# Kernel optimization log

Measured on AMD Instinct MI355X. Metric: run time of the kernel, lower is better.

The kernel has to match this reference:

```python
import jax, jax.numpy as jnp
import numpy as np

NUM_CLASSES = 1000
FEATURE_DIM = 1024
BATCH = 8192
MOMENTUM = 0.9
LAMBDA_INTRA = 1.0
LAMBDA_INTER = 0.5


def setup_inputs() -> dict:
    key = jax.random.key(0)
    k1, k2, k3, k4 = jax.random.split(key, 4)
    return {
        "features": jax.random.normal(k1, (BATCH, FEATURE_DIM), jnp.float32),
        "features_adv": jax.random.normal(k2, (BATCH, FEATURE_DIM), jnp.float32),
        "centers": jax.random.normal(k3, (NUM_CLASSES, FEATURE_DIM), jnp.float32),
        "labels": jax.random.randint(k4, (BATCH,), 0, NUM_CLASSES, dtype=jnp.int64),
    }


def _l2_normalize(x):
    # torch F.normalize(p=2, dim=1) with eps=1e-12 clamp on the norm
    n = jnp.linalg.norm(x, axis=1, keepdims=True)
    return x / jnp.maximum(n, 1e-12)


def _update_centers(centers, feats, labels):
    # Vectorized version of the per-class masked-mean momentum update.
    C = centers.shape[0]
    sums = jax.ops.segment_sum(feats, labels, num_segments=C)            # [C, D]
    counts = jax.ops.segment_sum(jnp.ones((feats.shape[0],), feats.dtype), labels, num_segments=C)  # [C]
    means = sums / jnp.maximum(counts, 1.0)[:, None]
    has_samples = (counts > 0)[:, None]
    center_is_zero = jnp.all(centers == 0, axis=1, keepdims=True)
    updated = jnp.where(center_is_zero, means, MOMENTUM * centers + (1.0 - MOMENTUM) * means)
    return jnp.where(has_samples, updated, centers)


def reference(features, features_adv, centers, labels):
    f = _l2_normalize(features)
    fa = _l2_normalize(features_adv)

    # update_centers runs under no_grad on detached normalized features
    centers_new = _update_centers(centers, jax.lax.stop_gradient(f), labels)

    centers_batch = centers_new[labels]  # [B, D] gather
    intra_clean = jnp.linalg.norm(f - centers_batch, axis=1).mean()
    intra_adv = jnp.linalg.norm(fa - centers_batch, axis=1).mean()

    # fused pairwise center distances: ||ci||^2 + ||cj||^2 - 2 ci.cj
    sq = jnp.sum(centers_new * centers_new, axis=1)                      # [C]
    d2 = sq[:, None] + sq[None, :] - 2.0 * (centers_new @ centers_new.T)  # [C, C]
    dist = jnp.sqrt(jnp.maximum(d2, 0.0))
    C = centers_new.shape[0]
    upper = jnp.triu(jnp.ones((C, C), dtype=bool), k=1)
    n_pairs = C * (C - 1) / 2.0
    inter_loss = jnp.sum(jnp.where(upper, jax.nn.relu(1.0 - dist), 0.0)) / n_pairs

    return LAMBDA_INTRA * (intra_clean + intra_adv) - LAMBDA_INTER * inter_loss
```

## Files before the change

kernel.cpp:

```cpp
#include <hip/hip_runtime.h>
#include <math.h>

#define BATCH 8192
#define DIM 1024
#define NCLS 1000
#define NPAD 1024
#define NPAIRS 499500.0f
#define INTER_TILES 136
#define MAXROWS 128

typedef float  f32x4  __attribute__((ext_vector_type(4)));
typedef short  bf16x8 __attribute__((ext_vector_type(8)));


__device__ inline float waveAllReduceAdd(float x) {
  #pragma unroll
  for (int m = 32; m > 0; m >>= 1) x += __shfl_xor(x, m);
  return x;
}

__device__ inline float blockReduce1(float x, float* sm) {
  x = waveAllReduceAdd(x);
  int lane = threadIdx.x & 63, wid = threadIdx.x >> 6;
  __syncthreads();
  if (lane == 0) sm[wid] = x;
  __syncthreads();
  return sm[0] + sm[1] + sm[2] + sm[3];
}

__device__ inline unsigned short f2bf(float f) {
  unsigned int u = __float_as_uint(f);
  u += 0x7FFFu + ((u >> 16) & 1u);
  return (unsigned short)(u >> 16);
}

__device__ inline void gload_lds16(const float* g, float* l) {
  __builtin_amdgcn_global_load_lds(
      (const __attribute__((address_space(1))) void*)g,
      (__attribute__((address_space(3))) void*)l, 16, 0, 0);
}

__device__ inline void waitvm0() {
  asm volatile("s_waitcnt vmcnt(0)" ::: "memory");
}

__device__ inline void cfence() { asm volatile("" ::: "memory"); }


__global__ __launch_bounds__(256, 4)
void center_intra_kernel(const float* __restrict__ feats,
                         const float* __restrict__ featsa,
                         const float* __restrict__ centers,
                         const int* __restrict__ labels,
                         unsigned short* __restrict__ centers_bf,
                         float* __restrict__ sqn,
                         float* __restrict__ pclean,
                         float* __restrict__ padv) {
  __shared__ float  s_stage[4][DIM];
  __shared__ float4 s_accf[4][256];
  __shared__ float4 s_c4[256];
  __shared__ float  s_iw[MAXROWS];
  __shared__ int    s_rows[MAXROWS];
  __shared__ int    s_cnt;
  __shared__ int    s_anynz;
  __shared__ float  sm[8];

  int c = blockIdx.x;
  int tid = threadIdx.x;
  int lane = tid & 63, w = tid >> 6;
  int fi = tid;

  if (c >= NCLS) {
    ((ushort4*)(centers_bf + (size_t)c * DIM))[fi] = make_ushort4(0, 0, 0, 0);
    return;
  }

  if (tid == 0) { s_cnt = 0; s_anynz = 0; }
  __syncthreads();
  #pragma unroll 4
  for (int j = tid; j < BATCH; j += 256) {
    if (labels[j] == c) {
      int p = atomicAdd(&s_cnt, 1);
      if (p < MAXROWS) s_rows[p] = j;
    }
  }
  __syncthreads();
  int n = min(s_cnt, MAXROWS);

  float4 acc[4];
  #pragma unroll
  for (int i = 0; i < 4; ++i) acc[i] = make_float4(0.f, 0.f, 0.f, 0.f);
  float* myst = s_stage[w];

  for (int t = w; t < n; t += 4) {
    int r = s_rows[t];
    const float* src = feats + (size_t)r * DIM;
    #pragma unroll
    for (int q = 0; q < 4; ++q)
      gload_lds16(src + q * 256 + lane * 4, myst + q * 256);
    waitvm0();
    float4 v[4];
    #pragma unroll
    for (int i = 0; i < 4; ++i) v[i] = ((const float4*)myst)[lane + 64 * i];
    float ss = 0.f;
    #pragma unroll
    for (int i = 0; i < 4; ++i)
      ss += v[i].x * v[i].x + v[i].y * v[i].y + v[i].z * v[i].z + v[i].w * v[i].w;
    ss = waveAllReduceAdd(ss);
    float iw = 1.0f / fmaxf(sqrtf(ss), 1e-12f);
    if (lane == 0) s_iw[t] = iw;
    #pragma unroll
    for (int i = 0; i < 4; ++i) {
      acc[i].x += v[i].x * iw; acc[i].y += v[i].y * iw;
      acc[i].z += v[i].z * iw; acc[i].w += v[i].w * iw;
    }
    cfence();
  }

  #pragma unroll
  for (int i = 0; i < 4; ++i) s_accf[w][lane + 64 * i] = acc[i];
  float4 cv = ((const float4*)(centers + (size_t)c * DIM))[fi];
  if (cv.x != 0.f || cv.y != 0.f || cv.z != 0.f || cv.w != 0.f) s_anynz = 1;
  __syncthreads();
  float4 a0 = s_accf[0][fi], a1 = s_accf[1][fi], a2 = s_accf[2][fi], a3 = s_accf[3][fi];
  float4 sum = make_float4(a0.x + a1.x + a2.x + a3.x, a0.y + a1.y + a2.y + a3.y,
                           a0.z + a1.z + a2.z + a3.z, a0.w + a1.w + a2.w + a3.w);

  float invc = 1.0f / fmaxf((float)n, 1.0f);
  float4 mean = make_float4(sum.x * invc, sum.y * invc, sum.z * invc, sum.w * invc);

  float4 o;
  if (s_anynz) {
    o = make_float4(0.9f * cv.x + 0.1f * mean.x, 0.9f * cv.y + 0.1f * mean.y,
                    0.9f * cv.z + 0.1f * mean.z, 0.9f * cv.w + 0.1f * mean.w);
  } else {
    o = mean;
  }
  if (n == 0) o = cv;

  ((ushort4*)(centers_bf + (size_t)c * DIM))[fi] =
      make_ushort4(f2bf(o.x), f2bf(o.y), f2bf(o.z), f2bf(o.w));
  s_c4[fi] = o;

  float sq = blockReduce1(o.x * o.x + o.y * o.y + o.z * o.z + o.w * o.w, sm);
  if (tid == 0) sqn[c] = sq;

  float sumc = 0.f, suma = 0.f;
  for (int t = w; t < n; t += 4) {
    int r = s_rows[t];
    const float4* rp = (const float4*)(feats  + (size_t)r * DIM);
    const float4* ap = (const float4*)(featsa + (size_t)r * DIM);
    float dotf = 0.f, dota = 0.f, ssa = 0.f;
    #pragma unroll
    for (int i = 0; i < 4; ++i) {
      float4 vf = rp[lane + 64 * i];
      float4 va = ap[lane + 64 * i];
      float4 cc = s_c4[lane + 64 * i];
      dotf += vf.x * cc.x + vf.y * cc.y + vf.z * cc.z + vf.w * cc.w;
      dota += va.x * cc.x + va.y * cc.y + va.z * cc.z + va.w * cc.w;
      ssa  += va.x * va.x + va.y * va.y + va.z * va.z + va.w * va.w;
    }
    dotf = waveAllReduceAdd(dotf);
    dota = waveAllReduceAdd(dota);
    ssa  = waveAllReduceAdd(ssa);
    if (lane == 0) {
      float iw = s_iw[t];
      float inva = 1.0f / fmaxf(sqrtf(ssa), 1e-12f);
      float d2c = 1.0f + sq - 2.0f * iw * dotf;
      float d2a = 1.0f + sq - 2.0f * inva * dota;
      sumc += sqrtf(fmaxf(d2c, 0.0f));
      suma += sqrtf(fmaxf(d2a, 0.0f));
    }
  }

  float totc = blockReduce1(sumc, sm);
  float tota = blockReduce1(suma, sm);
  if (tid == 0) { pclean[c] = totc; padv[c] = tota; }
}


__global__ __launch_bounds__(256, 4)
void inter_mfma_kernel(const unsigned short* __restrict__ Cbf,
                       const float* __restrict__ sq,
                       float* __restrict__ pinter) {
  __shared__ float smr[8];
  int tid = threadIdx.x;
  int bid = blockIdx.x;

  int t = bid;
  int bi = 0;
  while (t >= 16 - bi) { t -= 16 - bi; ++bi; }
  int bj = bi + t;

  int w = tid >> 6;
  int wy = w >> 1, wx = w & 1;
  int lane = tid & 63;
  int m = lane & 15;
  int q = lane >> 4;

  int i0 = bi * 64 + wy * 32;
  int j0 = bj * 64 + wx * 32;

  const unsigned short* arow0 = Cbf + (size_t)(i0 + m) * DIM;
  const unsigned short* arow1 = Cbf + (size_t)(i0 + 16 + m) * DIM;
  const unsigned short* brow0 = Cbf + (size_t)(j0 + m) * DIM;
  const unsigned short* brow1 = Cbf + (size_t)(j0 + 16 + m) * DIM;

  f32x4 acc00 = {0.f, 0.f, 0.f, 0.f}, acc01 = acc00, acc10 = acc00, acc11 = acc00;

  #pragma unroll 4
  for (int k0 = 0; k0 < DIM; k0 += 32) {
    int ko = k0 + q * 8;
    bf16x8 a0 = *(const bf16x8*)(arow0 + ko);
    bf16x8 a1 = *(const bf16x8*)(arow1 + ko);
    bf16x8 b0 = *(const bf16x8*)(brow0 + ko);
    bf16x8 b1 = *(const bf16x8*)(brow1 + ko);
    acc00 = __builtin_amdgcn_mfma_f32_16x16x32_bf16(a0, b0, acc00, 0, 0, 0);
    acc01 = __builtin_amdgcn_mfma_f32_16x16x32_bf16(a0, b1, acc01, 0, 0, 0);
    acc10 = __builtin_amdgcn_mfma_f32_16x16x32_bf16(a1, b0, acc10, 0, 0, 0);
    acc11 = __builtin_amdgcn_mfma_f32_16x16x32_bf16(a1, b1, acc11, 0, 0, 0);
  }

  float local = 0.f;
  int colA = lane & 15;
  int rbase = (lane >> 4) * 4;
  #pragma unroll
  for (int si = 0; si < 2; ++si) {
    #pragma unroll
    for (int sj = 0; sj < 2; ++sj) {
      f32x4 a = (si == 0) ? (sj == 0 ? acc00 : acc01) : (sj == 0 ? acc10 : acc11);
      #pragma unroll
      for (int r = 0; r < 4; ++r) {
        int i = i0 + si * 16 + rbase + r;
        int j = j0 + sj * 16 + colA;
        if (j < NCLS && i < j) {
          float d2 = sq[i] + sq[j] - 2.0f * a[r];
          float d = sqrtf(fmaxf(d2, 0.0f));
          local += fmaxf(1.0f - d, 0.0f);
        }
      }
    }
  }
  float tot = blockReduce1(local, smr);
  if (tid == 0) pinter[bid] = tot;
}


__global__ void final_kernel(const float* __restrict__ pclean,
                             const float* __restrict__ padv,
                             const float* __restrict__ pinter,
                             float* __restrict__ out) {
  __shared__ float sm[8];
  int t = threadIdx.x;
  float ci = 0.f;
  for (int i = t; i < NCLS; i += 256) ci += pclean[i] + padv[i];
  float e = (t < INTER_TILES) ? pinter[t] : 0.f;
  ci = blockReduce1(ci, sm);
  e = blockReduce1(e, sm);
  if (t == 0) {
    float intra = ci * (1.0f / (float)BATCH);
    float inter = e / NPAIRS;
    out[0] = intra - 0.5f * inter;
  }
}


extern "C" void kernel_launch(void* const* d_in, const int* in_sizes, int n_in,
                              void* d_out, int out_size, void* d_ws, size_t ws_size,
                              hipStream_t stream) {
  const float* features     = (const float*)d_in[0];
  const float* features_adv = (const float*)d_in[1];
  const float* centers      = (const float*)d_in[2];
  const int*   labels       = (const int*)d_in[3];
  float* out = (float*)d_out;

  unsigned short* centers_bf = (unsigned short*)d_ws;
  float* sqn = (float*)(centers_bf + (size_t)NPAD * DIM);
  float* pclean = sqn + 1024;
  float* padv = pclean + 1024;
  float* pinter = padv + 1024;

  hipLaunchKernelGGL(center_intra_kernel, dim3(NPAD), dim3(256), 0, stream,
                     features, features_adv, centers, labels, centers_bf, sqn,
                     pclean, padv);
  hipLaunchKernelGGL(inter_mfma_kernel, dim3(INTER_TILES), dim3(256), 0, stream,
                     centers_bf, sqn, pinter);
  hipLaunchKernelGGL(final_kernel, dim3(1), dim3(256), 0, stream, pclean, padv,
                     pinter, out);
}
```

Measured before the change: 138.7 us.

## Double-buffer feature row loads into LDS and vectorize label scan

Adds per-wave double-buffered LDS staging so the next feature row is prefetched with global_load_lds while the current row is reduced, using a partial vmcnt wait. The second pass streams adversarial rows the same way through LDS instead of direct global loads. The label scan now reads labels as int4. The goal is to hide global memory latency in the per-class gather. In exchange, LDS use per block doubles for the staging buffers (the old accumulator array now reuses them), which may lower occupancy. The hand-written vmcnt counting is fragile because the second loop also issues plain global loads.

```diff
diff --git a/kernel.cpp b/kernel.cpp
--- a/kernel.cpp
+++ b/kernel.cpp
@@ -43,7 +43,9 @@
 __device__ inline void waitvm0() {
   asm volatile("s_waitcnt vmcnt(0)" ::: "memory");
 }
-
+__device__ inline void waitvm4() {
+  asm volatile("s_waitcnt vmcnt(4)" ::: "memory");
+}
 __device__ inline void cfence() { asm volatile("" ::: "memory"); }
 
 
@@ -56,8 +58,7 @@
                          float* __restrict__ sqn,
                          float* __restrict__ pclean,
                          float* __restrict__ padv) {
-  __shared__ float  s_stage[4][DIM];
-  __shared__ float4 s_accf[4][256];
+  __shared__ float  s_stage[8][DIM];
   __shared__ float4 s_c4[256];
   __shared__ float  s_iw[MAXROWS];
   __shared__ int    s_rows[MAXROWS];
@@ -77,31 +78,44 @@
 
   if (tid == 0) { s_cnt = 0; s_anynz = 0; }
   __syncthreads();
-  #pragma unroll 4
-  for (int j = tid; j < BATCH; j += 256) {
-    if (labels[j] == c) {
-      int p = atomicAdd(&s_cnt, 1);
-      if (p < MAXROWS) s_rows[p] = j;
-    }
+  const int4* lab4 = (const int4*)labels;
+  #pragma unroll 2
+  for (int j = tid; j < BATCH / 4; j += 256) {
+    int4 lv = lab4[j];
+    if (lv.x == c) { int p = atomicAdd(&s_cnt, 1); if (p < MAXROWS) s_rows[p] = 4 * j; }
+    if (lv.y == c) { int p = atomicAdd(&s_cnt, 1); if (p < MAXROWS) s_rows[p] = 4 * j + 1; }
+    if (lv.z == c) { int p = atomicAdd(&s_cnt, 1); if (p < MAXROWS) s_rows[p] = 4 * j + 2; }
+    if (lv.w == c) { int p = atomicAdd(&s_cnt, 1); if (p < MAXROWS) s_rows[p] = 4 * j + 3; }
   }
   __syncthreads();
   int n = min(s_cnt, MAXROWS);
+
+  float* bufA = s_stage[2 * w];
+  float* bufB = s_stage[2 * w + 1];
 
   float4 acc[4];
   #pragma unroll
   for (int i = 0; i < 4; ++i) acc[i] = make_float4(0.f, 0.f, 0.f, 0.f);
-  float* myst = s_stage[w];
-
+
+  if (w < n) {
+    const float* src = feats + (size_t)s_rows[w] * DIM;
+    #pragma unroll
+    for (int q = 0; q < 4; ++q) gload_lds16(src + q * 256 + lane * 4, bufA + q * 256);
+  }
   for (int t = w; t < n; t += 4) {
-    int r = s_rows[t];
-    const float* src = feats + (size_t)r * DIM;
-    #pragma unroll
-    for (int q = 0; q < 4; ++q)
-      gload_lds16(src + q * 256 + lane * 4, myst + q * 256);
-    waitvm0();
+    int tn = t + 4;
+    if (tn < n) {
+      const float* src = feats + (size_t)s_rows[tn] * DIM;
+      #pragma unroll
+      for (int q = 0; q < 4; ++q) gload_lds16(src + q * 256 + lane * 4, bufB + q * 256);
+      cfence();
+      waitvm4();
+    } else {
+      waitvm0();
+    }
     float4 v[4];
     #pragma unroll
-    for (int i = 0; i < 4; ++i) v[i] = ((const float4*)myst)[lane + 64 * i];
+    for (int i = 0; i < 4; ++i) v[i] = ((const float4*)bufA)[lane + 64 * i];
     float ss = 0.f;
     #pragma unroll
     for (int i = 0; i < 4; ++i)
@@ -115,14 +129,17 @@
       acc[i].z += v[i].z * iw; acc[i].w += v[i].w * iw;
     }
     cfence();
-  }
-
+    float* tmp = bufA; bufA = bufB; bufB = tmp;
+  }
+
+  __syncthreads();
   #pragma unroll
-  for (int i = 0; i < 4; ++i) s_accf[w][lane + 64 * i] = acc[i];
+  for (int i = 0; i < 4; ++i) ((float4*)s_stage[w])[lane + 64 * i] = acc[i];
   float4 cv = ((const float4*)(centers + (size_t)c * DIM))[fi];
   if (cv.x != 0.f || cv.y != 0.f || cv.z != 0.f || cv.w != 0.f) s_anynz = 1;
   __syncthreads();
-  float4 a0 = s_accf[0][fi], a1 = s_accf[1][fi], a2 = s_accf[2][fi], a3 = s_accf[3][fi];
+  float4 a0 = ((const float4*)s_stage[0])[fi], a1 = ((const float4*)s_stage[1])[fi];
+  float4 a2 = ((const float4*)s_stage[2])[fi], a3 = ((const float4*)s_stage[3])[fi];
   float4 sum = make_float4(a0.x + a1.x + a2.x + a3.x, a0.y + a1.y + a2.y + a3.y,
                            a0.z + a1.z + a2.z + a3.z, a0.w + a1.w + a2.w + a3.w);
 
@@ -145,18 +162,38 @@
   float sq = blockReduce1(o.x * o.x + o.y * o.y + o.z * o.z + o.w * o.w, sm);
   if (tid == 0) sqn[c] = sq;
 
+  bufA = s_stage[2 * w];
+  bufB = s_stage[2 * w + 1];
   float sumc = 0.f, suma = 0.f;
+
+  if (w < n) {
+    const float* src = featsa + (size_t)s_rows[w] * DIM;
+    #pragma unroll
+    for (int q = 0; q < 4; ++q) gload_lds16(src + q * 256 + lane * 4, bufA + q * 256);
+  }
   for (int t = w; t < n; t += 4) {
     int r = s_rows[t];
-    const float4* rp = (const float4*)(feats  + (size_t)r * DIM);
-    const float4* ap = (const float4*)(featsa + (size_t)r * DIM);
+    const float4* rp = (const float4*)(feats + (size_t)r * DIM);
+    float4 vf[4];
+    #pragma unroll
+    for (int i = 0; i < 4; ++i) vf[i] = rp[lane + 64 * i];
+    cfence();
+    int tn = t + 4;
+    if (tn < n) {
+      const float* src = featsa + (size_t)s_rows[tn] * DIM;
+      #pragma unroll
+      for (int q = 0; q < 4; ++q) gload_lds16(src + q * 256 + lane * 4, bufB + q * 256);
+      cfence();
+      waitvm4();
+    } else {
+      waitvm0();
+    }
     float dotf = 0.f, dota = 0.f, ssa = 0.f;
     #pragma unroll
     for (int i = 0; i < 4; ++i) {
-      float4 vf = rp[lane + 64 * i];
-      float4 va = ap[lane + 64 * i];
+      float4 va = ((const float4*)bufA)[lane + 64 * i];
       float4 cc = s_c4[lane + 64 * i];
-      dotf += vf.x * cc.x + vf.y * cc.y + vf.z * cc.z + vf.w * cc.w;
+      dotf += vf[i].x * cc.x + vf[i].y * cc.y + vf[i].z * cc.z + vf[i].w * cc.w;
       dota += va.x * cc.x + va.y * cc.y + va.z * cc.z + va.w * cc.w;
       ssa  += va.x * va.x + va.y * va.y + va.z * va.z + va.w * va.w;
     }
@@ -171,6 +208,8 @@
       sumc += sqrtf(fmaxf(d2c, 0.0f));
       suma += sqrtf(fmaxf(d2a, 0.0f));
     }
+    cfence();
+    float* tmp = bufA; bufA = bufB; bufB = tmp;
   }
 
   float totc = blockReduce1(sumc, sm);
```

Result: faster. 134.3 us (-3.2%).
